# Performance work log

Hardware: AMD Instinct MI355X
Metric: run time of the kernel (lower is better)

## Reference

```python
import jax, jax.numpy as jnp
import numpy as np

N_NODES = 100000
N_EDGES = 3200000
EMB = 256
OUT = 256


def setup_inputs() -> dict:
    key = jax.random.key(0)
    k1, k2, k3, k4, k5 = jax.random.split(key, 5)
    embeddings = jax.random.normal(k1, (N_NODES, EMB), dtype=jnp.float32)
    adj_rows = jax.random.randint(k2, (N_EDGES,), 0, N_NODES, dtype=jnp.int32)
    adj_cols = jax.random.randint(k3, (N_EDGES,), 0, N_NODES, dtype=jnp.int32)
    adj_vals = jax.random.uniform(k4, (N_EDGES,), dtype=jnp.float32)
    W = jax.random.normal(k5, (EMB, OUT), dtype=jnp.float32) * 0.02
    return {
        "embeddings": embeddings,
        "adj_rows": adj_rows,
        "adj_cols": adj_cols,
        "adj_vals": adj_vals,
        "W": W,
    }


def reference(embeddings, adj_rows, adj_cols, adj_vals, W):
    # SpMM: agg[i] = sum_{e: rows[e]==i} vals[e] * embeddings[cols[e]]
    messages = adj_vals[:, None] * embeddings[adj_cols]  # [E, EMB]
    agg = jax.ops.segment_sum(messages, adj_rows, num_segments=embeddings.shape[0])  # [N, EMB]
    # Dense projection + ReLU
    out = jax.nn.relu(agg @ W)  # [N, OUT]
    return out
```

## Files before the change

### kernel.cpp

```cpp
#include <hip/hip_runtime.h>
#include <stdint.h>


typedef unsigned short u16;
typedef __attribute__((ext_vector_type(8))) short short8v;
typedef __attribute__((ext_vector_type(4))) float f32x4;

#define RBSH 6
#define RB 64
#define NBMAX 2048
#define MS_T 4096
#define MS_PT 16

__device__ __forceinline__ float b2f(u16 u) {
  union { unsigned i; float f; } x; x.i = ((unsigned)u) << 16; return x.f;
}
__device__ __forceinline__ u16 f2b(float f) {
  union { unsigned i; float f; } x; x.f = f;
  unsigned r = x.i + 0x7fffu + ((x.i >> 16) & 1u);
  return (u16)(r >> 16);
}

__global__ void detect_k(const unsigned* __restrict__ valsw, int* __restrict__ flag) {
  __shared__ int cnt;
  if (threadIdx.x == 0) cnt = 0;
  __syncthreads();
  int c = 0;
  for (int i = threadIdx.x; i < 4096; i += 256) {
    unsigned w = valsw[i];
    if ((w & 0xFFFFu) >= 0x3F80u) c++;
  }
  atomicAdd(&cnt, c);
  __syncthreads();
  if (threadIdx.x == 0) *flag = (cnt < 1024) ? 1 : 0;
}

__global__ __launch_bounds__(256) void bhist_k(const int* __restrict__ rows,
                                               int* __restrict__ bcounts, int E, int NB) {
  __shared__ int h[NBMAX];
  int tid = threadIdx.x;
  for (int b = tid; b < NB; b += 256) h[b] = 0;
  __syncthreads();
  for (int i = blockIdx.x * 256 + tid; i < E; i += gridDim.x * 256)
    atomicAdd(&h[rows[i] >> RBSH], 1);
  __syncthreads();
  for (int b = tid; b < NB; b += 256) {
    int c = h[b];
    if (c) atomicAdd(&bcounts[b], c);
  }
}

__global__ __launch_bounds__(256) void bscan_k(const int* __restrict__ bcounts,
                                               int* __restrict__ boffs,
                                               int* __restrict__ bcursor, int NB) {
  __shared__ int part[256];
  int tid = threadIdx.x;
  int K = (NB + 255) >> 8;
  int lo = tid * K, hi = lo + K;
  if (hi > NB) hi = NB;
  if (lo > NB) lo = NB;
  int s = 0;
  for (int b = lo; b < hi; ++b) s += bcounts[b];
  part[tid] = s;
  __syncthreads();
  for (int o = 1; o < 256; o <<= 1) {
    int v = (tid >= o) ? part[tid - o] : 0;
    __syncthreads();
    part[tid] += v;
    __syncthreads();
  }
  int run = part[tid] - s;
  for (int b = lo; b < hi; ++b) {
    int c = bcounts[b];
    boffs[b] = run;
    bcursor[b] = run;
    run += c;
  }
  if (tid == 255) boffs[NB] = part[255];
}

template <bool BF16>
__global__ __launch_bounds__(256) void ms_k(const int* __restrict__ flag,
                                            const int* __restrict__ rows,
                                            const int* __restrict__ cols,
                                            const void* __restrict__ valsv,
                                            int* __restrict__ bcursor,
                                            int2* __restrict__ pack, int E, int NB) {
  if (*flag != (BF16 ? 1 : 0)) return;
  __shared__ int hist[NBMAX + 1];
  __shared__ int gbase[NBMAX];
  __shared__ int part[256];
  __shared__ int2 buf[MS_T];
  __shared__ u16 brow[MS_T];
  int tid = threadIdx.x;
  int base = blockIdx.x * MS_T;

  for (int b = tid; b <= NB; b += 256) hist[b] = 0;
  __syncthreads();

  int bk[MS_PT], ofs[MS_PT], cl[MS_PT], vb[MS_PT];
#pragma unroll
  for (int i = 0; i < MS_PT; ++i) {
    int e = base + i * 256 + tid;
    if (e < E) {
      int r = rows[e];
      bk[i] = r >> RBSH;
      cl[i] = cols[e] | ((r & (RB - 1)) << 17);
      float v = BF16 ? b2f(((const u16*)valsv)[e]) : ((const float*)valsv)[e];
      vb[i] = __float_as_int(v);
      ofs[i] = atomicAdd(&hist[bk[i]], 1);
    } else {
      bk[i] = -1; ofs[i] = 0; cl[i] = 0; vb[i] = 0;
    }
  }
  __syncthreads();

  int K = (NB + 255) >> 8;
  int lo = tid * K, hi = lo + K;
  if (hi > NB) hi = NB;
  if (lo > NB) lo = NB;
  int s = 0;
  for (int b = lo; b < hi; ++b) s += hist[b];
  part[tid] = s;
  __syncthreads();
  for (int o = 1; o < 256; o <<= 1) {
    int v = (tid >= o) ? part[tid - o] : 0;
    __syncthreads();
    part[tid] += v;
    __syncthreads();
  }
  int run = part[tid] - s;
  for (int b = lo; b < hi; ++b) {
    int c = hist[b];
    hist[b] = run;
    run += c;
  }
  if (tid == 255) hist[NB] = part[255];
  __syncthreads();

#pragma unroll
  for (int i = 0; i < MS_PT; ++i) {
    if (bk[i] >= 0) {
      int slot = hist[bk[i]] + ofs[i];
      buf[slot] = make_int2(cl[i], vb[i]);
      brow[slot] = (u16)bk[i];
    }
  }
  for (int b = tid; b < NB; b += 256) {
    int c = hist[b + 1] - hist[b];
    if (c > 0) gbase[b] = atomicAdd(&bcursor[b], c);
  }
  __syncthreads();

  int tot = hist[NB];
  for (int i = tid; i < tot; i += 256) {
    int b = brow[i];
    pack[gbase[b] + (i - hist[b])] = buf[i];
  }
}

__global__ __launch_bounds__(256) void ms2_k(const int* __restrict__ boffs,
                                             const int2* __restrict__ pack,
                                             int2* __restrict__ pack2,
                                             int* __restrict__ offs, int N, int NB) {
  __shared__ int bins[RB];
  __shared__ int pfx[RB];
  int b = blockIdx.x;
  int tid = threadIdx.x;
  int beg = boffs[b], end = boffs[b + 1];
  if (tid < RB) bins[tid] = 0;
  __syncthreads();
  for (int i = beg + tid; i < end; i += 256)
    atomicAdd(&bins[(pack[i].x >> 17) & (RB - 1)], 1);
  __syncthreads();
  if (tid == 0) {
    int run = 0;
    for (int r = 0; r < RB; ++r) { int c = bins[r]; pfx[r] = run; run += c; }
  }
  __syncthreads();
  if (tid < RB) {
    int n = b * RB + tid;
    if (n < N) offs[n] = beg + pfx[tid];
    bins[tid] = pfx[tid];
  }
  if (b == NB - 1 && tid == 0) offs[N] = end;
  __syncthreads();
  for (int i = beg + tid; i < end; i += 256) {
    int2 q = pack[i];
    int r = (q.x >> 17) & (RB - 1);
    int p = atomicAdd(&bins[r], 1);
    pack2[beg + p] = q;
  }
}

template <bool BF16>
__global__ void wtr_k(const int* __restrict__ flag, const void* __restrict__ Wv,
                      u16* __restrict__ Wt) {
  if (*flag != (BF16 ? 1 : 0)) return;
  int i = blockIdx.x * 256 + threadIdx.x;
  int n = i >> 8, k = i & 255;
  float w = BF16 ? b2f(((const u16*)Wv)[k * 256 + n]) : ((const float*)Wv)[k * 256 + n];
  Wt[n * 256 + k] = f2b(w);
}

template <bool BF16>
__global__ __launch_bounds__(256) void proj_k(const int* __restrict__ flag,
                                              const void* __restrict__ embv,
                                              const u16* __restrict__ Wt,
                                              u16* __restrict__ P, int N) {
  if (*flag != (BF16 ? 1 : 0)) return;
  int wave = threadIdx.x >> 6, lane = threadIdx.x & 63;
  int lr = lane & 15, lq = lane >> 4;
  int m0 = blockIdx.x * 64;
  int n0 = wave * 64;

  f32x4 acc[4][4];
#pragma unroll
  for (int mi = 0; mi < 4; ++mi)
#pragma unroll
    for (int ni = 0; ni < 4; ++ni) acc[mi][ni] = (f32x4)0.f;

  int arow[4];
#pragma unroll
  for (int mi = 0; mi < 4; ++mi) {
    int r = m0 + mi * 16 + lr;
    arow[mi] = r < N ? r : N - 1;
  }

  for (int ks = 0; ks < 8; ++ks) {
    int kb = ks * 32 + lq * 8;
    short8v a[4], b[4];
#pragma unroll
    for (int mi = 0; mi < 4; ++mi) {
      if (BF16) {
        a[mi] = *(const short8v*)((const u16*)embv + (size_t)arow[mi] * 256 + kb);
      } else {
        const float* p = (const float*)embv + (size_t)arow[mi] * 256 + kb;
        float4 x = *(const float4*)p;
        float4 y = *(const float4*)(p + 4);
        short8v t;
        t[0] = (short)f2b(x.x); t[1] = (short)f2b(x.y);
        t[2] = (short)f2b(x.z); t[3] = (short)f2b(x.w);
        t[4] = (short)f2b(y.x); t[5] = (short)f2b(y.y);
        t[6] = (short)f2b(y.z); t[7] = (short)f2b(y.w);
        a[mi] = t;
      }
    }
#pragma unroll
    for (int ni = 0; ni < 4; ++ni)
      b[ni] = *(const short8v*)(Wt + (size_t)(n0 + ni * 16 + lr) * 256 + kb);
#pragma unroll
    for (int mi = 0; mi < 4; ++mi)
#pragma unroll
      for (int ni = 0; ni < 4; ++ni)
        acc[mi][ni] = __builtin_amdgcn_mfma_f32_16x16x32_bf16(a[mi], b[ni], acc[mi][ni], 0, 0, 0);
  }

#pragma unroll
  for (int mi = 0; mi < 4; ++mi) {
    int rbase = m0 + mi * 16 + lq * 4;
#pragma unroll
    for (int ni = 0; ni < 4; ++ni) {
      int col = n0 + ni * 16 + lr;
#pragma unroll
      for (int r = 0; r < 4; ++r) {
        int row = rbase + r;
        if (row < N) P[(size_t)row * 256 + col] = f2b(acc[mi][ni][r]);
      }
    }
  }
}

template <bool OUTBF16>
__global__ __launch_bounds__(256) void agg_k(const int* __restrict__ flag,
                                             const u16* __restrict__ P,
                                             const int* __restrict__ offs,
                                             const int2* __restrict__ pack,
                                             void* __restrict__ outv, int N) {
  if (*flag != (OUTBF16 ? 1 : 0)) return;
  int wave = threadIdx.x >> 6, lane = threadIdx.x & 63;
  int node = blockIdx.x * 4 + wave;
  if (node >= N) return;
  int beg = offs[node], end = offs[node + 1];
  float a0 = 0.f, a1 = 0.f, a2 = 0.f, a3 = 0.f;
  const u16* pb = P + lane * 4;
  int j = beg;
  for (; j + 8 <= end; j += 8) {
    int2 q0 = pack[j + 0], q1 = pack[j + 1], q2 = pack[j + 2], q3 = pack[j + 3];
    int2 q4 = pack[j + 4], q5 = pack[j + 5], q6 = pack[j + 6], q7 = pack[j + 7];
    ushort4 e0 = *(const ushort4*)(pb + (size_t)(q0.x & 0x1FFFF) * 256);
    ushort4 e1 = *(const ushort4*)(pb + (size_t)(q1.x & 0x1FFFF) * 256);
    ushort4 e2 = *(const ushort4*)(pb + (size_t)(q2.x & 0x1FFFF) * 256);
    ushort4 e3 = *(const ushort4*)(pb + (size_t)(q3.x & 0x1FFFF) * 256);
    ushort4 e4 = *(const ushort4*)(pb + (size_t)(q4.x & 0x1FFFF) * 256);
    ushort4 e5 = *(const ushort4*)(pb + (size_t)(q5.x & 0x1FFFF) * 256);
    ushort4 e6 = *(const ushort4*)(pb + (size_t)(q6.x & 0x1FFFF) * 256);
    ushort4 e7 = *(const ushort4*)(pb + (size_t)(q7.x & 0x1FFFF) * 256);
    float v0 = __int_as_float(q0.y), v1 = __int_as_float(q1.y);
    float v2 = __int_as_float(q2.y), v3 = __int_as_float(q3.y);
    float v4 = __int_as_float(q4.y), v5 = __int_as_float(q5.y);
    float v6 = __int_as_float(q6.y), v7 = __int_as_float(q7.y);
    a0 += v0 * b2f(e0.x); a1 += v0 * b2f(e0.y); a2 += v0 * b2f(e0.z); a3 += v0 * b2f(e0.w);
    a0 += v1 * b2f(e1.x); a1 += v1 * b2f(e1.y); a2 += v1 * b2f(e1.z); a3 += v1 * b2f(e1.w);
    a0 += v2 * b2f(e2.x); a1 += v2 * b2f(e2.y); a2 += v2 * b2f(e2.z); a3 += v2 * b2f(e2.w);
    a0 += v3 * b2f(e3.x); a1 += v3 * b2f(e3.y); a2 += v3 * b2f(e3.z); a3 += v3 * b2f(e3.w);
    a0 += v4 * b2f(e4.x); a1 += v4 * b2f(e4.y); a2 += v4 * b2f(e4.z); a3 += v4 * b2f(e4.w);
    a0 += v5 * b2f(e5.x); a1 += v5 * b2f(e5.y); a2 += v5 * b2f(e5.z); a3 += v5 * b2f(e5.w);
    a0 += v6 * b2f(e6.x); a1 += v6 * b2f(e6.y); a2 += v6 * b2f(e6.z); a3 += v6 * b2f(e6.w);
    a0 += v7 * b2f(e7.x); a1 += v7 * b2f(e7.y); a2 += v7 * b2f(e7.z); a3 += v7 * b2f(e7.w);
  }
  for (; j < end; ++j) {
    int2 q = pack[j];
    float v = __int_as_float(q.y);
    ushort4 e = *(const ushort4*)(pb + (size_t)(q.x & 0x1FFFF) * 256);
    a0 += v * b2f(e.x); a1 += v * b2f(e.y); a2 += v * b2f(e.z); a3 += v * b2f(e.w);
  }
  a0 = fmaxf(a0, 0.f); a1 = fmaxf(a1, 0.f);
  a2 = fmaxf(a2, 0.f); a3 = fmaxf(a3, 0.f);
  if (OUTBF16) {
    ushort4 o; o.x = f2b(a0); o.y = f2b(a1); o.z = f2b(a2); o.w = f2b(a3);
    *(ushort4*)((u16*)outv + (size_t)node * 256 + lane * 4) = o;
  } else {
    float4 o; o.x = a0; o.y = a1; o.z = a2; o.w = a3;
    *(float4*)((float*)outv + (size_t)node * 256 + lane * 4) = o;
  }
}


extern "C" void kernel_launch(void* const* d_in, const int* in_sizes, int n_in,
                              void* d_out, int out_size, void* d_ws, size_t ws_size,
                              hipStream_t stream) {
  const void* emb  = d_in[0];
  const int*  rows = (const int*)d_in[1];
  const int*  cols = (const int*)d_in[2];
  const void* vals = d_in[3];
  const void* W    = d_in[4];

  int N = in_sizes[0] / 256;
  int E = in_sizes[1];
  int NB = (N + RB - 1) >> RBSH;

  char* ws = (char*)d_ws;
  size_t off = 0;
  auto carve = [&](size_t bytes) -> char* {
    char* p = ws + off;
    off += (bytes + 511) & ~(size_t)511;
    return p;
  };
  int*  flag    = (int*) carve(4);
  int*  bcounts = (int*) carve((size_t)NBMAX * 4);
  int*  boffs   = (int*) carve((size_t)(NBMAX + 1) * 4);
  int*  bcursor = (int*) carve((size_t)NBMAX * 4);
  int*  offs    = (int*) carve((size_t)(N + 1) * 4);
  int2* pack    = (int2*)carve((size_t)E * 8);
  int2* pack2   = (int2*)carve((size_t)E * 8);
  u16*  P       = (u16*) carve((size_t)N * 256 * 2);
  u16*  Wt      = (u16*) carve((size_t)256 * 256 * 2);
  (void)ws_size; (void)n_in; (void)out_size;

  hipMemsetAsync(bcounts, 0, (size_t)NBMAX * 4, stream);

  detect_k<<<1, 256, 0, stream>>>((const unsigned*)vals, flag);

  bhist_k<<<256, 256, 0, stream>>>(rows, bcounts, E, NB);
  bscan_k<<<1, 256, 0, stream>>>(bcounts, boffs, bcursor, NB);

  wtr_k<true ><<<256, 256, 0, stream>>>(flag, W, Wt);
  wtr_k<false><<<256, 256, 0, stream>>>(flag, W, Wt);

  int pb = (N + 63) / 64;
  proj_k<true ><<<pb, 256, 0, stream>>>(flag, emb, Wt, P, N);
  proj_k<false><<<pb, 256, 0, stream>>>(flag, emb, Wt, P, N);

  int mb = (E + MS_T - 1) / MS_T;
  ms_k<true ><<<mb, 256, 0, stream>>>(flag, rows, cols, vals, bcursor, pack, E, NB);
  ms_k<false><<<mb, 256, 0, stream>>>(flag, rows, cols, vals, bcursor, pack, E, NB);

  ms2_k<<<NB, 256, 0, stream>>>(boffs, pack, pack2, offs, N, NB);

  int ab = (N + 3) / 4;
  agg_k<true ><<<ab, 256, 0, stream>>>(flag, P, offs, pack2, d_out, N);
  agg_k<false><<<ab, 256, 0, stream>>>(flag, P, offs, pack2, d_out, N);
}
```

Measured before the change: 592.5 us.

## Use deterministic per-block bucket offsets, wider buckets, and 16-byte gathers in aggregation

The bucket sort now has each tile write its own per-bucket histogram, and a single-block scan computes every tile's global base. This removes the global atomic cursor from the scatter kernel and makes edge placement deterministic. The bucket width grows from 64 to 256 rows, so there are fewer buckets and larger second-pass bins, and the second pass now uses a parallel scan. The aggregation kernel has each half-wave load 16 bytes of a projected row per edge and handle alternate edges, then combines the halves with a shuffle, aiming for better memory-level parallelism. The trade-offs are a serial per-bucket loop over all tiles in the scan kernel and wasted lanes when a node has few edges.

```diff
diff --git a/kernel.cpp b/kernel.cpp
--- a/kernel.cpp
+++ b/kernel.cpp
@@ -6,9 +6,9 @@
 typedef __attribute__((ext_vector_type(8))) short short8v;
 typedef __attribute__((ext_vector_type(4))) float f32x4;
 
-#define RBSH 6
-#define RB 64
-#define NBMAX 2048
+#define RBSH 8
+#define RB 256
+#define NBMAX 512
 #define MS_T 4096
 #define MS_PT 16
 
@@ -20,6 +20,12 @@
   unsigned r = x.i + 0x7fffu + ((x.i >> 16) & 1u);
   return (u16)(r >> 16);
 }
+__device__ __forceinline__ float blo(unsigned u) {
+  union { unsigned i; float f; } x; x.i = u << 16; return x.f;
+}
+__device__ __forceinline__ float bhi(unsigned u) {
+  union { unsigned i; float f; } x; x.i = u & 0xFFFF0000u; return x.f;
+}
 
 __global__ void detect_k(const unsigned* __restrict__ valsw, int* __restrict__ flag) {
   __shared__ int cnt;
@@ -35,57 +41,58 @@
   if (threadIdx.x == 0) *flag = (cnt < 1024) ? 1 : 0;
 }
 
-__global__ __launch_bounds__(256) void bhist_k(const int* __restrict__ rows,
-                                               int* __restrict__ bcounts, int E, int NB) {
+__global__ __launch_bounds__(256) void count_k(const int* __restrict__ rows,
+                                               int* __restrict__ cnt, int E, int NB) {
   __shared__ int h[NBMAX];
   int tid = threadIdx.x;
   for (int b = tid; b < NB; b += 256) h[b] = 0;
   __syncthreads();
-  for (int i = blockIdx.x * 256 + tid; i < E; i += gridDim.x * 256)
-    atomicAdd(&h[rows[i] >> RBSH], 1);
-  __syncthreads();
-  for (int b = tid; b < NB; b += 256) {
-    int c = h[b];
-    if (c) atomicAdd(&bcounts[b], c);
-  }
-}
-
-__global__ __launch_bounds__(256) void bscan_k(const int* __restrict__ bcounts,
+  int base = blockIdx.x * MS_T;
+#pragma unroll
+  for (int i = 0; i < MS_PT; ++i) {
+    int e = base + i * 256 + tid;
+    if (e < E) atomicAdd(&h[rows[e] >> RBSH], 1);
+  }
+  __syncthreads();
+  for (int b = tid; b < NB; b += 256) cnt[(size_t)blockIdx.x * NB + b] = h[b];
+}
+
+__global__ __launch_bounds__(512) void mscan_k(int* __restrict__ cnt,
                                                int* __restrict__ boffs,
-                                               int* __restrict__ bcursor, int NB) {
-  __shared__ int part[256];
+                                               int NB, int NBLK) {
+  __shared__ int part[512];
   int tid = threadIdx.x;
-  int K = (NB + 255) >> 8;
-  int lo = tid * K, hi = lo + K;
-  if (hi > NB) hi = NB;
-  if (lo > NB) lo = NB;
-  int s = 0;
-  for (int b = lo; b < hi; ++b) s += bcounts[b];
-  part[tid] = s;
-  __syncthreads();
-  for (int o = 1; o < 256; o <<= 1) {
+  int tot = 0;
+  if (tid < NB)
+    for (int blk = 0; blk < NBLK; ++blk) tot += cnt[(size_t)blk * NB + tid];
+  part[tid] = (tid < NB) ? tot : 0;
+  __syncthreads();
+  for (int o = 1; o < 512; o <<= 1) {
     int v = (tid >= o) ? part[tid - o] : 0;
     __syncthreads();
     part[tid] += v;
     __syncthreads();
   }
-  int run = part[tid] - s;
-  for (int b = lo; b < hi; ++b) {
-    int c = bcounts[b];
-    boffs[b] = run;
-    bcursor[b] = run;
-    run += c;
-  }
-  if (tid == 255) boffs[NB] = part[255];
+  if (tid < NB) {
+    int run = part[tid] - tot;
+    boffs[tid] = run;
+    for (int blk = 0; blk < NBLK; ++blk) {
+      size_t idx = (size_t)blk * NB + tid;
+      int c = cnt[idx];
+      cnt[idx] = run;
+      run += c;
+    }
+  }
+  if (tid == 511) boffs[NB] = part[511];
 }
 
 template <bool BF16>
-__global__ __launch_bounds__(256) void ms_k(const int* __restrict__ flag,
-                                            const int* __restrict__ rows,
-                                            const int* __restrict__ cols,
-                                            const void* __restrict__ valsv,
-                                            int* __restrict__ bcursor,
-                                            int2* __restrict__ pack, int E, int NB) {
+__global__ __launch_bounds__(256) void place_k(const int* __restrict__ flag,
+                                               const int* __restrict__ rows,
+                                               const int* __restrict__ cols,
+                                               const void* __restrict__ valsv,
+                                               const int* __restrict__ base,
+                                               int2* __restrict__ pack, int E, int NB) {
   if (*flag != (BF16 ? 1 : 0)) return;
   __shared__ int hist[NBMAX + 1];
   __shared__ int gbase[NBMAX];
@@ -93,15 +100,16 @@
   __shared__ int2 buf[MS_T];
   __shared__ u16 brow[MS_T];
   int tid = threadIdx.x;
-  int base = blockIdx.x * MS_T;
+  int tbase = blockIdx.x * MS_T;
 
   for (int b = tid; b <= NB; b += 256) hist[b] = 0;
+  for (int b = tid; b < NB; b += 256) gbase[b] = base[(size_t)blockIdx.x * NB + b];
   __syncthreads();
 
   int bk[MS_PT], ofs[MS_PT], cl[MS_PT], vb[MS_PT];
 #pragma unroll
   for (int i = 0; i < MS_PT; ++i) {
-    int e = base + i * 256 + tid;
+    int e = tbase + i * 256 + tid;
     if (e < E) {
       int r = rows[e];
       bk[i] = r >> RBSH;
@@ -146,10 +154,6 @@
       brow[slot] = (u16)bk[i];
     }
   }
-  for (int b = tid; b < NB; b += 256) {
-    int c = hist[b + 1] - hist[b];
-    if (c > 0) gbase[b] = atomicAdd(&bcursor[b], c);
-  }
   __syncthreads();
 
   int tot = hist[NB];
@@ -164,26 +168,30 @@
                                              int2* __restrict__ pack2,
                                              int* __restrict__ offs, int N, int NB) {
   __shared__ int bins[RB];
-  __shared__ int pfx[RB];
+  __shared__ int part[256];
   int b = blockIdx.x;
   int tid = threadIdx.x;
   int beg = boffs[b], end = boffs[b + 1];
-  if (tid < RB) bins[tid] = 0;
+  bins[tid] = 0;
   __syncthreads();
   for (int i = beg + tid; i < end; i += 256)
     atomicAdd(&bins[(pack[i].x >> 17) & (RB - 1)], 1);
   __syncthreads();
-  if (tid == 0) {
-    int run = 0;
-    for (int r = 0; r < RB; ++r) { int c = bins[r]; pfx[r] = run; run += c; }
-  }
-  __syncthreads();
-  if (tid < RB) {
-    int n = b * RB + tid;
-    if (n < N) offs[n] = beg + pfx[tid];
-    bins[tid] = pfx[tid];
-  }
+  int c = bins[tid];
+  part[tid] = c;
+  __syncthreads();
+  for (int o = 1; o < 256; o <<= 1) {
+    int v = (tid >= o) ? part[tid - o] : 0;
+    __syncthreads();
+    part[tid] += v;
+    __syncthreads();
+  }
+  int pfx = part[tid] - c;
+  __syncthreads();
+  int n = b * RB + tid;
+  if (n < N) offs[n] = beg + pfx;
   if (b == NB - 1 && tid == 0) offs[N] = end;
+  bins[tid] = pfx;
   __syncthreads();
   for (int i = beg + tid; i < end; i += 256) {
     int2 q = pack[i];
@@ -281,48 +289,46 @@
   int wave = threadIdx.x >> 6, lane = threadIdx.x & 63;
   int node = blockIdx.x * 4 + wave;
   if (node >= N) return;
+  int sub = lane & 31, half = lane >> 5;
   int beg = offs[node], end = offs[node + 1];
-  float a0 = 0.f, a1 = 0.f, a2 = 0.f, a3 = 0.f;
-  const u16* pb = P + lane * 4;
-  int j = beg;
-  for (; j + 8 <= end; j += 8) {
-    int2 q0 = pack[j + 0], q1 = pack[j + 1], q2 = pack[j + 2], q3 = pack[j + 3];
-    int2 q4 = pack[j + 4], q5 = pack[j + 5], q6 = pack[j + 6], q7 = pack[j + 7];
-    ushort4 e0 = *(const ushort4*)(pb + (size_t)(q0.x & 0x1FFFF) * 256);
-    ushort4 e1 = *(const ushort4*)(pb + (size_t)(q1.x & 0x1FFFF) * 256);
-    ushort4 e2 = *(const ushort4*)(pb + (size_t)(q2.x & 0x1FFFF) * 256);
-    ushort4 e3 = *(const ushort4*)(pb + (size_t)(q3.x & 0x1FFFF) * 256);
-    ushort4 e4 = *(const ushort4*)(pb + (size_t)(q4.x & 0x1FFFF) * 256);
-    ushort4 e5 = *(const ushort4*)(pb + (size_t)(q5.x & 0x1FFFF) * 256);
-    ushort4 e6 = *(const ushort4*)(pb + (size_t)(q6.x & 0x1FFFF) * 256);
-    ushort4 e7 = *(const ushort4*)(pb + (size_t)(q7.x & 0x1FFFF) * 256);
-    float v0 = __int_as_float(q0.y), v1 = __int_as_float(q1.y);
-    float v2 = __int_as_float(q2.y), v3 = __int_as_float(q3.y);
-    float v4 = __int_as_float(q4.y), v5 = __int_as_float(q5.y);
-    float v6 = __int_as_float(q6.y), v7 = __int_as_float(q7.y);
-    a0 += v0 * b2f(e0.x); a1 += v0 * b2f(e0.y); a2 += v0 * b2f(e0.z); a3 += v0 * b2f(e0.w);
-    a0 += v1 * b2f(e1.x); a1 += v1 * b2f(e1.y); a2 += v1 * b2f(e1.z); a3 += v1 * b2f(e1.w);
-    a0 += v2 * b2f(e2.x); a1 += v2 * b2f(e2.y); a2 += v2 * b2f(e2.z); a3 += v2 * b2f(e2.w);
-    a0 += v3 * b2f(e3.x); a1 += v3 * b2f(e3.y); a2 += v3 * b2f(e3.z); a3 += v3 * b2f(e3.w);
-    a0 += v4 * b2f(e4.x); a1 += v4 * b2f(e4.y); a2 += v4 * b2f(e4.z); a3 += v4 * b2f(e4.w);
-    a0 += v5 * b2f(e5.x); a1 += v5 * b2f(e5.y); a2 += v5 * b2f(e5.z); a3 += v5 * b2f(e5.w);
-    a0 += v6 * b2f(e6.x); a1 += v6 * b2f(e6.y); a2 += v6 * b2f(e6.z); a3 += v6 * b2f(e6.w);
-    a0 += v7 * b2f(e7.x); a1 += v7 * b2f(e7.y); a2 += v7 * b2f(e7.z); a3 += v7 * b2f(e7.w);
-  }
-  for (; j < end; ++j) {
-    int2 q = pack[j];
-    float v = __int_as_float(q.y);
-    ushort4 e = *(const ushort4*)(pb + (size_t)(q.x & 0x1FFFF) * 256);
-    a0 += v * b2f(e.x); a1 += v * b2f(e.y); a2 += v * b2f(e.z); a3 += v * b2f(e.w);
-  }
-  a0 = fmaxf(a0, 0.f); a1 = fmaxf(a1, 0.f);
-  a2 = fmaxf(a2, 0.f); a3 = fmaxf(a3, 0.f);
+  const u16* pb = P + sub * 8;
+
+  float acc[8];
+#pragma unroll
+  for (int k = 0; k < 8; ++k) acc[k] = 0.f;
+
+  for (int j = beg; j < end; j += 16) {
+#pragma unroll
+    for (int k = 0; k < 8; ++k) {
+      int i0 = j + 2 * k + half;
+      int ic = i0 < end ? i0 : end - 1;
+      int2 q = pack[ic];
+      float v = i0 < end ? __int_as_float(q.y) : 0.f;
+      const int4* src = (const int4*)(pb + (size_t)(q.x & 0x1FFFF) * 256);
+      int4 u = *src;
+      acc[0] += v * blo((unsigned)u.x); acc[1] += v * bhi((unsigned)u.x);
+      acc[2] += v * blo((unsigned)u.y); acc[3] += v * bhi((unsigned)u.y);
+      acc[4] += v * blo((unsigned)u.z); acc[5] += v * bhi((unsigned)u.z);
+      acc[6] += v * blo((unsigned)u.w); acc[7] += v * bhi((unsigned)u.w);
+    }
+  }
+
+#pragma unroll
+  for (int k = 0; k < 8; ++k) acc[k] += __shfl(acc[k], lane ^ 32);
+
+#pragma unroll
+  for (int k = 0; k < 8; ++k) acc[k] = fmaxf(acc[k], 0.f);
+  int d0 = sub * 8 + half * 4;
   if (OUTBF16) {
-    ushort4 o; o.x = f2b(a0); o.y = f2b(a1); o.z = f2b(a2); o.w = f2b(a3);
-    *(ushort4*)((u16*)outv + (size_t)node * 256 + lane * 4) = o;
+    ushort4 o;
+    o.x = f2b(acc[half * 4 + 0]); o.y = f2b(acc[half * 4 + 1]);
+    o.z = f2b(acc[half * 4 + 2]); o.w = f2b(acc[half * 4 + 3]);
+    *(ushort4*)((u16*)outv + (size_t)node * 256 + d0) = o;
   } else {
-    float4 o; o.x = a0; o.y = a1; o.z = a2; o.w = a3;
-    *(float4*)((float*)outv + (size_t)node * 256 + lane * 4) = o;
+    float4 o;
+    o.x = acc[half * 4 + 0]; o.y = acc[half * 4 + 1];
+    o.z = acc[half * 4 + 2]; o.w = acc[half * 4 + 3];
+    *(float4*)((float*)outv + (size_t)node * 256 + d0) = o;
   }
 }
 
@@ -339,6 +345,7 @@
   int N = in_sizes[0] / 256;
   int E = in_sizes[1];
   int NB = (N + RB - 1) >> RBSH;
+  int NBLK = (E + MS_T - 1) / MS_T;
 
   char* ws = (char*)d_ws;
   size_t off = 0;
@@ -347,23 +354,20 @@
     off += (bytes + 511) & ~(size_t)511;
     return p;
   };
-  int*  flag    = (int*) carve(4);
-  int*  bcounts = (int*) carve((size_t)NBMAX * 4);
-  int*  boffs   = (int*) carve((size_t)(NBMAX + 1) * 4);
-  int*  bcursor = (int*) carve((size_t)NBMAX * 4);
-  int*  offs    = (int*) carve((size_t)(N + 1) * 4);
-  int2* pack    = (int2*)carve((size_t)E * 8);
-  int2* pack2   = (int2*)carve((size_t)E * 8);
-  u16*  P       = (u16*) carve((size_t)N * 256 * 2);
-  u16*  Wt      = (u16*) carve((size_t)256 * 256 * 2);
+  int*  flag  = (int*) carve(4);
+  int*  cnt   = (int*) carve((size_t)NBLK * NB * 4);
+  int*  boffs = (int*) carve((size_t)(NB + 1) * 4);
+  int*  offs  = (int*) carve((size_t)(N + 1) * 4);
+  int2* pack  = (int2*)carve((size_t)E * 8);
+  int2* pack2 = (int2*)carve((size_t)E * 8);
+  u16*  P     = (u16*) carve((size_t)N * 256 * 2);
+  u16*  Wt    = (u16*) carve((size_t)256 * 256 * 2);
   (void)ws_size; (void)n_in; (void)out_size;
 
-  hipMemsetAsync(bcounts, 0, (size_t)NBMAX * 4, stream);
-
   detect_k<<<1, 256, 0, stream>>>((const unsigned*)vals, flag);
 
-  bhist_k<<<256, 256, 0, stream>>>(rows, bcounts, E, NB);
-  bscan_k<<<1, 256, 0, stream>>>(bcounts, boffs, bcursor, NB);
+  count_k<<<NBLK, 256, 0, stream>>>(rows, cnt, E, NB);
+  mscan_k<<<1, 512, 0, stream>>>(cnt, boffs, NB, NBLK);
 
   wtr_k<true ><<<256, 256, 0, stream>>>(flag, W, Wt);
   wtr_k<false><<<256, 256, 0, stream>>>(flag, W, Wt);
@@ -372,9 +376,8 @@
   proj_k<true ><<<pb, 256, 0, stream>>>(flag, emb, Wt, P, N);
   proj_k<false><<<pb, 256, 0, stream>>>(flag, emb, Wt, P, N);
 
-  int mb = (E + MS_T - 1) / MS_T;
-  ms_k<true ><<<mb, 256, 0, stream>>>(flag, rows, cols, vals, bcursor, pack, E, NB);
-  ms_k<false><<<mb, 256, 0, stream>>>(flag, rows, cols, vals, bcursor, pack, E, NB);
+  place_k<true ><<<NBLK, 256, 0, stream>>>(flag, rows, cols, vals, cnt, pack, E, NB);
+  place_k<false><<<NBLK, 256, 0, stream>>>(flag, rows, cols, vals, cnt, pack, E, NB);
 
   ms2_k<<<NB, 256, 0, stream>>>(boffs, pack, pack2, offs, N, NB);
 
```

Result: slower. 830.0 us (+40.1%).
